# Kernel optimization log

Measured on AMD Instinct MI355X. Metric: run time of the kernel, lower is better.

Reference implementation:

```python
import jax, jax.numpy as jnp
import numpy as np

B, S, IN, H = 64, 1024, 256, 512

def setup_inputs() -> dict:
    key = jax.random.key(0)
    ks = jax.random.split(key, 9)
    inputs = jax.random.normal(ks[0], (B, S, IN), dtype=jnp.float32)
    timestamps = jax.random.uniform(ks[1], (B, S), dtype=jnp.float32)
    input_lens = jax.random.randint(ks[2], (B,), 1, S + 1, dtype=jnp.int64)
    sc_h = 1.0 / np.sqrt(H)
    sc_i = 1.0 / np.sqrt(IN)
    # torch Linear: y = x @ W.T + b; store transposed weights [in, out]
    W_all = jax.random.uniform(ks[3], (H, 4 * H), jnp.float32, -sc_h, sc_h)
    b_all = jax.random.uniform(ks[4], (4 * H,), jnp.float32, -sc_h, sc_h)
    U_all = jax.random.uniform(ks[5], (IN, 4 * H), jnp.float32, -sc_i, sc_i)
    b_u = jax.random.uniform(ks[6], (4 * H,), jnp.float32, -sc_i, sc_i)
    W_d = jax.random.uniform(ks[7], (H, H), jnp.float32, -sc_h, sc_h)
    b_d = jax.random.uniform(ks[8], (H,), jnp.float32, -sc_h, sc_h)
    return {"inputs": inputs, "timestamps": timestamps, "input_lens": input_lens,
            "W_all": W_all, "b_all": b_all, "U_all": U_all, "b_u": b_u,
            "W_d": W_d, "b_d": b_d}

def _time_lstm(inputs, timestamps, input_lens, W_all, b_all, U_all, b_u, W_d, b_d):
    b = inputs.shape[0]
    hdim = W_d.shape[0]
    # precompute input projection once: [B,S,4H]
    x_proj = jnp.einsum('bsi,ig->bsg', inputs, U_all) + b_u
    # elapse gate: 1 / log(e + dt), [B,S,1]
    g = 1.0 / jnp.log(jnp.float32(np.e) + timestamps)

    def step(carry, xs):
        h, c = carry
        x_t, g_t = xs  # [B,4H], [B]
        c_s1 = jnp.tanh(c @ W_d + b_d)
        c_adj = c - c_s1 + c_s1 * g_t[:, None]
        outs = h @ W_all + b_all + x_t
        f, i, o, c_tmp = jnp.split(outs, 4, axis=1)
        c_new = jax.nn.sigmoid(f) * c_adj + jax.nn.sigmoid(i) * jnp.tanh(c_tmp)
        h_new = jax.nn.sigmoid(o) * jnp.tanh(c_new)
        return (h_new, c_new), (h_new, c_new)

    h0 = jnp.zeros((b, hdim), inputs.dtype)
    c0 = jnp.zeros((b, hdim), inputs.dtype)
    xs = (jnp.swapaxes(x_proj, 0, 1), jnp.swapaxes(g, 0, 1))  # time-major
    _, (h_seq, c_seq) = jax.lax.scan(step, (h0, c0), xs)
    h_seq = jnp.swapaxes(h_seq, 0, 1)  # [B,S,H]
    c_seq = jnp.swapaxes(c_seq, 0, 1)

    seq = inputs.shape[1]
    mask = (jnp.arange(seq)[None, :] < input_lens[:, None])  # [B,S]
    outputs = jnp.where(mask[:, :, None], h_seq, 0.0)  # zeros past length, like original
    last_idx = (input_lens - 1)[:, None, None]  # [B,1,1]
    last_h = jnp.take_along_axis(h_seq, jnp.broadcast_to(last_idx, (b, 1, hdim)), axis=1)[:, 0]
    last_c = jnp.take_along_axis(c_seq, jnp.broadcast_to(last_idx, (b, 1, hdim)), axis=1)[:, 0]
    return outputs, last_h, last_c

def reference(inputs, timestamps, input_lens, W_all, b_all, U_all, b_u, W_d, b_d):
    return _time_lstm(inputs, timestamps, input_lens, W_all, b_all, U_all, b_u, W_d, b_d)
```

## Files before the change

kernel.cpp:

```cpp
#include <hip/hip_runtime.h>


typedef _Float16 f16;
typedef _Float16 f16x8 __attribute__((ext_vector_type(8)));
typedef float f32x4 __attribute__((ext_vector_type(4)));

#define S_ 1024
#define IN_ 256
#define H_ 512
#define ECONST 2.718281828459045f

__device__ __forceinline__ float sigf(float x) { return 1.0f / (1.0f + __expf(-x)); }
__device__ __forceinline__ float tanh_f(float x) { return 1.0f - 2.0f / (__expf(2.0f * x) + 1.0f); }

__device__ __forceinline__ unsigned int pack_hc(float h, float c) {
    union { f16 f; unsigned short u; } ph, pc;
    ph.f = (f16)h; pc.f = (f16)c;
    return ((unsigned int)pc.u << 16) | (unsigned int)ph.u;
}

__launch_bounds__(320, 2)
__global__ void tlstm_scan(
    const float* __restrict__ inputs, const float* __restrict__ tstamps,
    const int* __restrict__ lens,
    const float* __restrict__ W_all, const float* __restrict__ b_all,
    const float* __restrict__ U_all, const float* __restrict__ b_u,
    const float* __restrict__ W_d, const float* __restrict__ b_d,
    float* __restrict__ out0, float* __restrict__ out1, float* __restrict__ out2,
    unsigned long long* __restrict__ hcbuf, unsigned int* __restrict__ flags)
{
    __shared__ __align__(16) f16 A_sm[96 * 16 * 8];
    __shared__ __align__(16) f16 C_sm[64 * 16 * 8];
    __shared__ float outs_sm[5 * 16 * 17];
    __shared__ float c_loc[16 * 16];
    __shared__ float bias_sm[5 * 16];
    __shared__ int   len_sm[16];

    const int tid    = threadIdx.x;
    const int grp    = blockIdx.x & 3;
    const int member = blockIdx.x >> 2;
    const int wave   = tid >> 6;
    const int lane   = tid & 63;
    const int q      = lane >> 4;
    const int r16    = lane & 15;
    const int j0     = member * 16;

    f16x8 bw[24];
    if (wave < 4) {
        const int col = wave * 512 + j0 + r16;
#pragma unroll
        for (int kk = 0; kk < 24; ++kk) {
            f16x8 v;
            const int kbase = kk * 32 + q * 8;
#pragma unroll
            for (int e = 0; e < 8; ++e) {
                const int k = kbase + e;
                const float w = (kk < 16) ? W_all[k * 2048 + col]
                                          : U_all[(k - 512) * 2048 + col];
                v[e] = (f16)w;
            }
            bw[kk] = v;
        }
    } else {
        const int col = j0 + r16;
#pragma unroll
        for (int kk = 0; kk < 16; ++kk) {
            f16x8 v;
            const int kbase = kk * 32 + q * 8;
#pragma unroll
            for (int e = 0; e < 8; ++e) v[e] = (f16)W_d[(kbase + e) * 512 + col];
            bw[kk] = v;
        }
#pragma unroll
        for (int kk = 16; kk < 24; ++kk) bw[kk] = bw[0];
    }

    int sl[7];
    int ns = 0;
    for (int s = wave; s < 32; s += 5)
        if (s != member) sl[ns++] = s;

    {
        uint4 z; z.x = z.y = z.z = z.w = 0u;
        uint4* a4 = (uint4*)A_sm;
        uint4* c4 = (uint4*)C_sm;
        for (int i = tid; i < 1024; i += 320) { a4[i] = z; c4[i] = z; }
        if (tid < 256) c_loc[tid] = 0.0f;
        if (tid < 64) {
            const int w = tid >> 4, n = tid & 15;
            const int col = w * 512 + j0 + n;
            bias_sm[w * 16 + n] = b_all[col] + b_u[col];
        } else if (tid < 80) {
            const int n = tid & 15;
            bias_sm[64 + n] = b_d[j0 + n];
        }
        if (tid < 16) len_sm[tid] = lens[grp * 16 + tid];
        for (int idx = tid; idx < 1024; idx += 320) {
            const int b = idx >> 6;
            const int kx0 = (idx & 63) << 2;
            const float4 v = *(const float4*)&inputs[(((size_t)(grp * 16 + b)) * S_ + 0) * IN_ + kx0];
            union { f16 h[4]; uint2 u; } p;
            p.h[0] = (f16)v.x; p.h[1] = (f16)v.y; p.h[2] = (f16)v.z; p.h[3] = (f16)v.w;
            const int kb = 64 + (kx0 >> 3), e = kx0 & 7;
            *(uint2*)&A_sm[(kb * 16 + b) * 8 + e] = p.u;
        }
    }
    __syncthreads();

    unsigned long long* const hc_g = hcbuf + (size_t)grp * 2 * 4096;
    unsigned int* const flg = flags + grp * 32;

    for (int t = 0; t < S_; ++t) {
        float ts = 0.0f;
        if (tid < 256) {
            const int gb = grp * 16 + (tid >> 4);
            ts = tstamps[(size_t)gb * S_ + t];
        }

        f32x4 acc0 = {0.f, 0.f, 0.f, 0.f}, acc1 = {0.f, 0.f, 0.f, 0.f};
        if (wave < 4) {
            const f16* abase = &A_sm[(q * 16 + r16) * 8];
#pragma unroll
            for (int kk = 0; kk < 24; ++kk) {
                const f16x8 a = *(const f16x8*)(abase + kk * 512);
                if (kk & 1) acc1 = __builtin_amdgcn_mfma_f32_16x16x32_f16(a, bw[kk], acc1, 0, 0, 0);
                else        acc0 = __builtin_amdgcn_mfma_f32_16x16x32_f16(a, bw[kk], acc0, 0, 0, 0);
            }
        } else {
            const f16* abase = &C_sm[(q * 16 + r16) * 8];
#pragma unroll
            for (int kk = 0; kk < 16; ++kk) {
                const f16x8 a = *(const f16x8*)(abase + kk * 512);
                if (kk & 1) acc1 = __builtin_amdgcn_mfma_f32_16x16x32_f16(a, bw[kk], acc1, 0, 0, 0);
                else        acc0 = __builtin_amdgcn_mfma_f32_16x16x32_f16(a, bw[kk], acc0, 0, 0, 0);
            }
        }
        const f32x4 acc = acc0 + acc1;
#pragma unroll
        for (int r = 0; r < 4; ++r)
            outs_sm[(wave * 16 + q * 4 + r) * 17 + r16] = acc[r];
        __syncthreads();

        if (tid < 256) {
            const int b = tid >> 4, jj = tid & 15;
            const int gb = grp * 16 + b;
            const float f  = outs_sm[(0 * 16 + b) * 17 + jj] + bias_sm[0  + jj];
            const float i_ = outs_sm[(1 * 16 + b) * 17 + jj] + bias_sm[16 + jj];
            const float o  = outs_sm[(2 * 16 + b) * 17 + jj] + bias_sm[32 + jj];
            const float ct = outs_sm[(3 * 16 + b) * 17 + jj] + bias_sm[48 + jj];
            const float d  = outs_sm[(4 * 16 + b) * 17 + jj] + bias_sm[64 + jj];
            const float gt = 1.0f / __logf(ECONST + ts);
            const float cs1   = tanh_f(d);
            const float cprev = c_loc[tid];
            const float cadj  = cprev - cs1 + cs1 * gt;
            const float cnew  = sigf(f) * cadj + sigf(i_) * tanh_f(ct);
            const float hnew  = sigf(o) * tanh_f(cnew);
            c_loc[tid] = cnew;
            const int col = j0 + jj;
            const int len = len_sm[b];
            out0[((size_t)gb * S_ + t) * H_ + col] = (t < len) ? hnew : 0.0f;
            if (t == len - 1) {
                out1[gb * H_ + col] = hnew;
                out2[gb * H_ + col] = cnew;
            }
            const int fi = ((col >> 3) * 16 + b) * 8 + (col & 7);
            ((f16*)A_sm)[fi] = (f16)hnew;
            ((f16*)C_sm)[fi] = (f16)cnew;
            unsigned int* dw = (unsigned int*)(hc_g + (size_t)(t & 1) * 4096);
            __hip_atomic_store(dw + member * 256 + tid, pack_hc(hnew, cnew),
                               __ATOMIC_RELAXED, __HIP_MEMORY_SCOPE_AGENT);
        }
        __syncthreads();

        if (t < S_ - 1) {
            const unsigned int tag = (unsigned int)(t + 1);
            if (tid == 0)
                __hip_atomic_store(&flg[member], tag,
                                   __ATOMIC_RELAXED, __HIP_MEMORY_SCOPE_AGENT);

            float4 xv[4];
            if (tid < 256) {
#pragma unroll
                for (int k2 = 0; k2 < 4; ++k2) {
                    const int idx = k2 * 256 + tid;
                    const int b = idx >> 6;
                    const int kx0 = (idx & 63) << 2;
                    xv[k2] = *(const float4*)&inputs[(((size_t)(grp * 16 + b)) * S_ + (t + 1)) * IN_ + kx0];
                }
            }

            for (;;) {
                unsigned int fl = tag;
                if (lane < ns)
                    fl = __hip_atomic_load(&flg[sl[lane]],
                                           __ATOMIC_RELAXED, __HIP_MEMORY_SCOPE_AGENT);
                if (__ballot(fl >= tag) == ~0ull) break;
            }

            const unsigned long long* src = hc_g + (size_t)(t & 1) * 4096;
            unsigned long long v[7][2];
#pragma unroll
            for (int u = 0; u < 7; ++u) {
                if (u < ns) {
                    const int s = sl[u];
                    v[u][0] = __hip_atomic_load(src + s * 128 + lane,
                                                __ATOMIC_RELAXED, __HIP_MEMORY_SCOPE_AGENT);
                    v[u][1] = __hip_atomic_load(src + s * 128 + 64 + lane,
                                                __ATOMIC_RELAXED, __HIP_MEMORY_SCOPE_AGENT);
                }
            }
#pragma unroll
            for (int u = 0; u < 7; ++u) {
                if (u < ns) {
                    const int s = sl[u];
#pragma unroll
                    for (int dd = 0; dd < 2; ++dd) {
                        const int j = dd * 64 + lane;
                        const int b = j >> 3;
                        const int colL = (j & 7) * 2;
                        const int col = s * 16 + colL;
                        const unsigned long long qv = v[u][dd];
                        const unsigned int d0 = (unsigned int)qv;
                        const unsigned int d1 = (unsigned int)(qv >> 32);
                        const unsigned int hpair = (d0 & 0xFFFFu) | (d1 << 16);
                        const unsigned int cpair = (d0 >> 16) | (d1 & 0xFFFF0000u);
                        const int fi = ((col >> 3) * 16 + b) * 8 + (col & 7);
                        *(unsigned int*)((f16*)A_sm + fi) = hpair;
                        *(unsigned int*)((f16*)C_sm + fi) = cpair;
                    }
                }
            }

            if (tid < 256) {
#pragma unroll
                for (int k2 = 0; k2 < 4; ++k2) {
                    const int idx = k2 * 256 + tid;
                    const int b = idx >> 6;
                    const int kx0 = (idx & 63) << 2;
                    union { f16 h[4]; uint2 u; } p;
                    p.h[0] = (f16)xv[k2].x; p.h[1] = (f16)xv[k2].y;
                    p.h[2] = (f16)xv[k2].z; p.h[3] = (f16)xv[k2].w;
                    const int kb = 64 + (kx0 >> 3), e = kx0 & 7;
                    *(uint2*)&A_sm[(kb * 16 + b) * 8 + e] = p.u;
                }
            }
            __syncthreads();
        }
    }
}

extern "C" void kernel_launch(void* const* d_in, const int* in_sizes, int n_in,
                              void* d_out, int out_size, void* d_ws, size_t ws_size,
                              hipStream_t stream) {
    const float* inputs  = (const float*)d_in[0];
    const float* tstamps = (const float*)d_in[1];
    const int*   lens    = (const int*)d_in[2];
    const float* W_all   = (const float*)d_in[3];
    const float* b_all   = (const float*)d_in[4];
    const float* U_all   = (const float*)d_in[5];
    const float* b_u     = (const float*)d_in[6];
    const float* W_d     = (const float*)d_in[7];
    const float* b_d     = (const float*)d_in[8];

    float* out0 = (float*)d_out;
    float* out1 = out0 + (size_t)64 * 1024 * 512;
    float* out2 = out1 + (size_t)64 * 512;

    char* ws = (char*)d_ws;
    unsigned int* flags = (unsigned int*)ws;
    unsigned long long* hcbuf = (unsigned long long*)(ws + 1024);

    hipMemsetAsync(ws, 0, 1024, stream);

    tlstm_scan<<<dim3(128), dim3(320), 0, stream>>>(
        inputs, tstamps, lens, W_all, b_all, U_all, b_u, W_d, b_d,
        out0, out1, out2, hcbuf, flags);
}
```

Baseline: 3.491 ms.

## Reorder step to publish h/c and flag before output stores; pipeline flag polling

The packed h/c value is now stored to the global exchange buffer right after it is computed, and the ready flag is raised before the out0/out1/out2 global stores, so peer blocks can proceed sooner. The next-step input load and fp16 conversion into shared memory now finish before the spin-wait instead of after it. The spin-wait keeps four outstanding flag loads in flight per watching lane to cut polling latency. The aim is to shorten the critical inter-block synchronization path of the recurrent scan. The cost is extra polling traffic and reliance on relaxed atomics with only a compiler barrier for ordering.

Measured after the change: 3.475 ms (median of 2 runs). Within noise of the previous version (-0.5%).

```diff
diff --git a/kernel.cpp b/kernel.cpp
--- a/kernel.cpp
+++ b/kernel.cpp
@@ -141,9 +141,9 @@
             outs_sm[(wave * 16 + q * 4 + r) * 17 + r16] = acc[r];
         __syncthreads();
 
+        float hnew_r = 0.0f, cnew_r = 0.0f;
         if (tid < 256) {
             const int b = tid >> 4, jj = tid & 15;
-            const int gb = grp * 16 + b;
             const float f  = outs_sm[(0 * 16 + b) * 17 + jj] + bias_sm[0  + jj];
             const float i_ = outs_sm[(1 * 16 + b) * 17 + jj] + bias_sm[16 + jj];
             const float o  = outs_sm[(2 * 16 + b) * 17 + jj] + bias_sm[32 + jj];
@@ -156,30 +156,37 @@
             const float cnew  = sigf(f) * cadj + sigf(i_) * tanh_f(ct);
             const float hnew  = sigf(o) * tanh_f(cnew);
             c_loc[tid] = cnew;
+            hnew_r = hnew; cnew_r = cnew;
+            unsigned int* dw = (unsigned int*)(hc_g + (size_t)(t & 1) * 4096);
+            __hip_atomic_store(dw + member * 256 + tid, pack_hc(hnew, cnew),
+                               __ATOMIC_RELAXED, __HIP_MEMORY_SCOPE_AGENT);
             const int col = j0 + jj;
-            const int len = len_sm[b];
-            out0[((size_t)gb * S_ + t) * H_ + col] = (t < len) ? hnew : 0.0f;
-            if (t == len - 1) {
-                out1[gb * H_ + col] = hnew;
-                out2[gb * H_ + col] = cnew;
-            }
             const int fi = ((col >> 3) * 16 + b) * 8 + (col & 7);
             ((f16*)A_sm)[fi] = (f16)hnew;
             ((f16*)C_sm)[fi] = (f16)cnew;
-            unsigned int* dw = (unsigned int*)(hc_g + (size_t)(t & 1) * 4096);
-            __hip_atomic_store(dw + member * 256 + tid, pack_hc(hnew, cnew),
+        }
+        __syncthreads();
+
+        const unsigned int tag = (unsigned int)(t + 1);
+        if (t < S_ - 1 && tid == 0)
+            __hip_atomic_store(&flg[member], tag,
                                __ATOMIC_RELAXED, __HIP_MEMORY_SCOPE_AGENT);
-        }
-        __syncthreads();
+
+        if (tid < 256) {
+            const int b = tid >> 4, jj = tid & 15;
+            const int gb = grp * 16 + b;
+            const int col = j0 + jj;
+            const int len = len_sm[b];
+            out0[((size_t)gb * S_ + t) * H_ + col] = (t < len) ? hnew_r : 0.0f;
+            if (t == len - 1) {
+                out1[gb * H_ + col] = hnew_r;
+                out2[gb * H_ + col] = cnew_r;
+            }
+        }
 
         if (t < S_ - 1) {
-            const unsigned int tag = (unsigned int)(t + 1);
-            if (tid == 0)
-                __hip_atomic_store(&flg[member], tag,
-                                   __ATOMIC_RELAXED, __HIP_MEMORY_SCOPE_AGENT);
-
-            float4 xv[4];
             if (tid < 256) {
+                float4 xv[4];
 #pragma unroll
                 for (int k2 = 0; k2 < 4; ++k2) {
                     const int idx = k2 * 256 + tid;
@@ -187,15 +194,38 @@
                     const int kx0 = (idx & 63) << 2;
                     xv[k2] = *(const float4*)&inputs[(((size_t)(grp * 16 + b)) * S_ + (t + 1)) * IN_ + kx0];
                 }
-            }
-
-            for (;;) {
-                unsigned int fl = tag;
-                if (lane < ns)
-                    fl = __hip_atomic_load(&flg[sl[lane]],
-                                           __ATOMIC_RELAXED, __HIP_MEMORY_SCOPE_AGENT);
-                if (__ballot(fl >= tag) == ~0ull) break;
-            }
+#pragma unroll
+                for (int k2 = 0; k2 < 4; ++k2) {
+                    const int idx = k2 * 256 + tid;
+                    const int b = idx >> 6;
+                    const int kx0 = (idx & 63) << 2;
+                    union { f16 h[4]; uint2 u; } p;
+                    p.h[0] = (f16)xv[k2].x; p.h[1] = (f16)xv[k2].y;
+                    p.h[2] = (f16)xv[k2].z; p.h[3] = (f16)xv[k2].w;
+                    const int kb = 64 + (kx0 >> 3), e = kx0 & 7;
+                    *(uint2*)&A_sm[(kb * 16 + b) * 8 + e] = p.u;
+                }
+            }
+
+            {
+                const bool watch = (lane < ns);
+                const unsigned int* fp = watch ? &flg[sl[lane]] : &flg[member];
+                unsigned int s0 = 0, s1 = 0, s2 = 0, s3 = 0;
+                if (watch) {
+                    s0 = __hip_atomic_load(fp, __ATOMIC_RELAXED, __HIP_MEMORY_SCOPE_AGENT);
+                    s1 = __hip_atomic_load(fp, __ATOMIC_RELAXED, __HIP_MEMORY_SCOPE_AGENT);
+                    s2 = __hip_atomic_load(fp, __ATOMIC_RELAXED, __HIP_MEMORY_SCOPE_AGENT);
+                    s3 = __hip_atomic_load(fp, __ATOMIC_RELAXED, __HIP_MEMORY_SCOPE_AGENT);
+                }
+                bool ok = !watch || (s0 >= tag);
+                while (__ballot(ok) != ~0ull) {
+                    s0 = s1; s1 = s2; s2 = s3;
+                    if (!ok)
+                        s3 = __hip_atomic_load(fp, __ATOMIC_RELAXED, __HIP_MEMORY_SCOPE_AGENT);
+                    ok = ok || (s0 >= tag);
+                }
+            }
+            asm volatile("" ::: "memory");
 
             const unsigned long long* src = hc_g + (size_t)(t & 1) * 4096;
             unsigned long long v[7][2];
@@ -230,20 +260,6 @@
                     }
                 }
             }
-
-            if (tid < 256) {
-#pragma unroll
-                for (int k2 = 0; k2 < 4; ++k2) {
-                    const int idx = k2 * 256 + tid;
-                    const int b = idx >> 6;
-                    const int kx0 = (idx & 63) << 2;
-                    union { f16 h[4]; uint2 u; } p;
-                    p.h[0] = (f16)xv[k2].x; p.h[1] = (f16)xv[k2].y;
-                    p.h[2] = (f16)xv[k2].z; p.h[3] = (f16)xv[k2].w;
-                    const int kb = 64 + (kx0 >> 3), e = kx0 & 7;
-                    *(uint2*)&A_sm[(kb * 16 + b) * 8 + e] = p.u;
-                }
-            }
             __syncthreads();
         }
     }
```
